# Kernel tuning notes

Measured on AMD Instinct MI355X. Metric: run time of the kernel, lower is better.

The kernel has to match this reference:

```python
import jax, jax.numpy as jnp
import numpy as np

THRESH = 0.5  # original code thresholds raw span logit channel 0 at 0.5


def setup_inputs() -> dict:
    key = jax.random.key(0)
    ks = jax.random.split(key, 9)
    B, S, H, P = 4, 256, 768, 54  # P = num_spo_patterns + 1
    scale = 0.02
    return {
        "sequence_output": jax.random.normal(ks[0], (B, S, H), jnp.float32),
        "W1s": jax.random.normal(ks[1], (H, H), jnp.float32) * scale,
        "b1s": jnp.zeros((H,), jnp.float32),
        "W2s": jax.random.normal(ks[2], (2, H), jnp.float32) * scale,
        "b2s": jnp.zeros((2,), jnp.float32),
        "Wp1": jax.random.normal(ks[3], (H, 2 * H), jnp.float32) * scale,
        "bp1": jnp.zeros((H,), jnp.float32),
        "Wp2": jax.random.normal(ks[4], (P, H), jnp.float32) * scale,
        "bp2": jnp.zeros((P,), jnp.float32),
    }


def reference(sequence_output, W1s, b1s, W2s, b2s, Wp1, bp1, Wp2, bp2):
    x = sequence_output                                # [B,S,H]
    B, S, H = x.shape
    # span classifier: Linear -> ReLU -> Linear
    h = jax.nn.relu(jnp.einsum('bsh,kh->bsk', x, W1s) + b1s)
    span_logits = jnp.einsum('bsh,kh->bsk', h, W2s) + b2s   # [B,S,2]
    cand = span_logits[..., 0] > THRESH                      # [B,S] candidates
    # spo pattern classifier on concat pairs: Linear(2H,H) splits into two H->H maps
    Wa, Wb = Wp1[:, :H], Wp1[:, H:]                          # subject / object halves
    ha = jnp.einsum('bsh,kh->bsk', x, Wa)                    # [B,S,H]
    hb = jnp.einsum('bsh,kh->bsk', x, Wb)                    # [B,S,H]
    pair_hidden = jax.nn.relu(ha[:, :, None, :] + hb[:, None, :, :] + bp1)  # [B,S,S,H]
    pair_logits = jnp.einsum('bijh,ph->bijp', pair_hidden, Wp2) + bp2       # [B,S,S,P]
    # valid pairs: both are candidates and subj != obj (diagonal excluded)
    not_diag = ~jnp.eye(S, dtype=bool)
    valid = cand[:, :, None] & cand[:, None, :] & not_diag   # [B,S,S]
    # dense masked equivalent of the per-pair Python loop (invalid pairs zeroed,
    # matching the zeros fallback for empty candidate sets)
    spo_pattern_logits = jnp.where(valid[..., None], pair_logits, 0.0)
    return spo_pattern_logits
```

## Files before the change

### kernel.cpp

```cpp
#include <hip/hip_runtime.h>
#include <hip/hip_bf16.h>


#define M_ROWS 1024
#define HDIM 768
#define PDIM 54
#define MAXC 256
#define KCHUNK 16
#define NKC (HDIM / KCHUNK)
#define KSPLIT 4
#define KSEG (HDIM / KSPLIT)

#define CANDCNT_OFF  0
#define PAIRCNT_OFF  4
#define CANDIDX_OFF  8192
#define CANDSLOT_OFF 12288
#define PAIR_OFF     16384
#define HPART_OFF    1064960

__global__ __launch_bounds__(256) void gemm_k_kernel(
    const float* __restrict__ x, const float* __restrict__ W1,
    float* __restrict__ hpart, int* __restrict__ counters)
{
    __shared__ float As[16][68];
    __shared__ float Bs[16][68];

    if (blockIdx.x == 0 && blockIdx.y == 0 && blockIdx.z == 0 && threadIdx.x < 2)
        counters[threadIdx.x] = 0;

    const int m0 = blockIdx.x * 64;
    const int n0 = blockIdx.y * 64;
    const int kb = blockIdx.z * KSEG;
    const int t  = threadIdx.x;
    const int tm = t & 15;
    const int tn = t >> 4;
    const int r  = t >> 2;
    const int c4 = (t & 3) * 4;

    float acc[4][4] = {};

    for (int k0 = kb; k0 < kb + KSEG; k0 += 16) {
        float4 av = *(const float4*)(x  + (size_t)(m0 + r) * HDIM + k0 + c4);
        float4 bv = *(const float4*)(W1 + (size_t)(n0 + r) * HDIM + k0 + c4);
        As[c4+0][r] = av.x; As[c4+1][r] = av.y; As[c4+2][r] = av.z; As[c4+3][r] = av.w;
        Bs[c4+0][r] = bv.x; Bs[c4+1][r] = bv.y; Bs[c4+2][r] = bv.z; Bs[c4+3][r] = bv.w;
        __syncthreads();
        #pragma unroll
        for (int kk = 0; kk < 16; ++kk) {
            float a[4], b[4];
            #pragma unroll
            for (int i = 0; i < 4; ++i) a[i] = As[kk][tm * 4 + i];
            #pragma unroll
            for (int j = 0; j < 4; ++j) b[j] = Bs[kk][tn * 4 + j];
            #pragma unroll
            for (int i = 0; i < 4; ++i)
                #pragma unroll
                for (int j = 0; j < 4; ++j)
                    acc[i][j] += a[i] * b[j];
        }
        __syncthreads();
    }

    float* dst = hpart + (size_t)blockIdx.z * (M_ROWS * HDIM);
    #pragma unroll
    for (int i = 0; i < 4; ++i) {
        float4 v = make_float4(acc[i][0], acc[i][1], acc[i][2], acc[i][3]);
        *(float4*)(dst + (size_t)(m0 + tm * 4 + i) * HDIM + n0 + tn * 4) = v;
    }
}

__global__ __launch_bounds__(256) void span_cand_kernel(
    const float* __restrict__ hpart, const float* __restrict__ b1,
    const float* __restrict__ w2row, const float* __restrict__ b2,
    int* __restrict__ candCount, int* __restrict__ candIdx,
    int* __restrict__ candSlot)
{
    const int m = blockIdx.x;
    const int t = threadIdx.x;
    float p = 0.f;
    for (int n = t; n < HDIM; n += 256) {
        float v = hpart[(size_t)m * HDIM + n]
                + hpart[(size_t)(M_ROWS * HDIM) + (size_t)m * HDIM + n]
                + hpart[(size_t)(2 * M_ROWS * HDIM) + (size_t)m * HDIM + n]
                + hpart[(size_t)(3 * M_ROWS * HDIM) + (size_t)m * HDIM + n];
        v += b1[n];
        v = v > 0.f ? v : 0.f;
        p += v * w2row[n];
    }
    __shared__ float wred[4];
    #pragma unroll
    for (int off = 32; off > 0; off >>= 1) p += __shfl_down(p, off, 64);
    if ((t & 63) == 0) wred[t >> 6] = p;
    __syncthreads();
    if (t == 0) {
        float s = wred[0] + wred[1] + wred[2] + wred[3] + b2[0];
        if (s > 0.5f) {
            int sl = atomicAdd(candCount, 1);
            if (sl < MAXC) { candIdx[sl] = m; candSlot[m] = sl; }
            else candSlot[m] = -1;
        } else {
            candSlot[m] = -1;
        }
    }
}

__global__ __launch_bounds__(256) void hab_kernel(
    const float* __restrict__ x, const float* __restrict__ Wp1,
    const int* __restrict__ candCount, const int* __restrict__ candIdx,
    float* __restrict__ ha, float* __restrict__ hb)
{
    __shared__ float xs[HDIM];
    __shared__ float red[2][KCHUNK][17];
    int nc = *candCount; if (nc > MAXC) nc = MAXC;
    const int nitems = nc * NKC;
    const int kk  = threadIdx.x >> 4;
    const int hb0 = (threadIdx.x & 15) * 4;

    for (int item = blockIdx.x; item < nitems; item += gridDim.x) {
        int slot = item / NKC;
        int kc   = item % NKC;
        int row  = candIdx[slot];

        for (int h = threadIdx.x; h < HDIM; h += 256)
            xs[h] = x[(size_t)row * HDIM + h];
        __syncthreads();

        int k = kc * KCHUNK + kk;
        const float* wr = Wp1 + (size_t)k * (2 * HDIM);
        float sa = 0.f, sb = 0.f;
        #pragma unroll
        for (int h = hb0; h < HDIM; h += 64) {
            float4 xv = *(const float4*)(xs + h);
            float4 wa = *(const float4*)(wr + h);
            float4 wb = *(const float4*)(wr + HDIM + h);
            sa += xv.x * wa.x + xv.y * wa.y + xv.z * wa.z + xv.w * wa.w;
            sb += xv.x * wb.x + xv.y * wb.y + xv.z * wb.z + xv.w * wb.w;
        }
        red[0][kk][threadIdx.x & 15] = sa;
        red[1][kk][threadIdx.x & 15] = sb;
        __syncthreads();

        if (threadIdx.x < 32) {
            int which = threadIdx.x >> 4;
            int kk2   = threadIdx.x & 15;
            float s = 0.f;
            #pragma unroll
            for (int g = 0; g < 16; ++g) s += red[which][kk2][g];
            float* dst = which == 0 ? ha : hb;
            dst[(size_t)slot * HDIM + kc * KCHUNK + kk2] = s;
        }
        __syncthreads();
    }
}

__global__ void pairs_kernel(const int* __restrict__ candSlot,
                             int* __restrict__ pairCount, int* __restrict__ pairList)
{
    int idx = blockIdx.x * 256 + threadIdx.x;
    int b = idx >> 16;
    int i = (idx >> 8) & 255;
    int j = idx & 255;
    if (i == j) return;
    if (candSlot[b * 256 + i] >= 0 && candSlot[b * 256 + j] >= 0) {
        int p = atomicAdd(pairCount, 1);
        pairList[p] = idx;
    }
}

__global__ __launch_bounds__(256) void pair_kernel(
    const float* __restrict__ ha, const float* __restrict__ hb,
    const float* __restrict__ bp1, const float* __restrict__ Wp2,
    const float* __restrict__ bp2, const int* __restrict__ candSlot,
    const int* __restrict__ pairCount, const int* __restrict__ pairList,
    float* __restrict__ out)
{
    __shared__ float v[HDIM];
    __shared__ float red[4][PDIM + 2];
    const int np = *pairCount;
    const int t = threadIdx.x;
    for (int p = blockIdx.x; p < np; p += gridDim.x) {
        int idx = pairList[p];
        int b = idx >> 16;
        int i = (idx >> 8) & 255;
        int j = idx & 255;
        int si = candSlot[b * 256 + i];
        int sj = candSlot[b * 256 + j];
        if (t < 192) {
            float4 a4 = *(const float4*)(ha + (size_t)si * HDIM + t * 4);
            float4 b4 = *(const float4*)(hb + (size_t)sj * HDIM + t * 4);
            float4 c4 = *(const float4*)(bp1 + t * 4);
            float4 r;
            r.x = a4.x + b4.x + c4.x; r.x = r.x > 0.f ? r.x : 0.f;
            r.y = a4.y + b4.y + c4.y; r.y = r.y > 0.f ? r.y : 0.f;
            r.z = a4.z + b4.z + c4.z; r.z = r.z > 0.f ? r.z : 0.f;
            r.w = a4.w + b4.w + c4.w; r.w = r.w > 0.f ? r.w : 0.f;
            *(float4*)(v + t * 4) = r;
        }
        __syncthreads();
        if (t < 216) {
            int pp  = t % PDIM;
            int seg = t / PDIM;
            const float* w = Wp2 + (size_t)pp * HDIM + seg * 192;
            const float* vv = v + seg * 192;
            float s = 0.f;
            for (int h = 0; h < 192; h += 4) {
                float4 a = *(const float4*)(vv + h);
                float4 b2_ = *(const float4*)(w + h);
                s += a.x * b2_.x + a.y * b2_.y + a.z * b2_.z + a.w * b2_.w;
            }
            red[seg][pp] = s;
        }
        __syncthreads();
        if (t < PDIM)
            out[(size_t)idx * PDIM + t] = red[0][t] + red[1][t] + red[2][t] + red[3][t] + bp2[t];
        __syncthreads();
    }
}

extern "C" void kernel_launch(void* const* d_in, const int* in_sizes, int n_in,
                              void* d_out, int out_size, void* d_ws, size_t ws_size,
                              hipStream_t stream) {
    const float* x   = (const float*)d_in[0];
    const float* W1s = (const float*)d_in[1];
    const float* b1s = (const float*)d_in[2];
    const float* W2s = (const float*)d_in[3];
    const float* b2s = (const float*)d_in[4];
    const float* Wp1 = (const float*)d_in[5];
    const float* bp1 = (const float*)d_in[6];
    const float* Wp2 = (const float*)d_in[7];
    const float* bp2 = (const float*)d_in[8];

    char* ws = (char*)d_ws;
    int*   counters = (int*)(ws + CANDCNT_OFF);
    int*   candCnt  = counters;
    int*   pairCnt  = counters + 1;
    int*   candIdx  = (int*)(ws + CANDIDX_OFF);
    int*   candSlot = (int*)(ws + CANDSLOT_OFF);
    int*   pairList = (int*)(ws + PAIR_OFF);
    float* hpart    = (float*)(ws + HPART_OFF);
    float* ha       = hpart + (size_t)KSPLIT * M_ROWS * HDIM;
    float* hb       = ha + (size_t)MAXC * HDIM;
    float* out = (float*)d_out;

    hipMemsetAsync(out, 0, (size_t)out_size * sizeof(float), stream);

    dim3 g(M_ROWS / 64, HDIM / 64, KSPLIT);
    gemm_k_kernel<<<g, 256, 0, stream>>>(x, W1s, hpart, counters);

    span_cand_kernel<<<M_ROWS, 256, 0, stream>>>(hpart, b1s, W2s, b2s,
                                                 candCnt, candIdx, candSlot);

    hab_kernel<<<2048, 256, 0, stream>>>(x, Wp1, candCnt, candIdx, ha, hb);

    pairs_kernel<<<1024, 256, 0, stream>>>(candSlot, pairCnt, pairList);

    pair_kernel<<<512, 256, 0, stream>>>(ha, hb, bp1, Wp2, bp2,
                                         candSlot, pairCnt, pairList, out);
}
```

Measured before the change: 138.9 us.

## Fuse pair enumeration and output zeroing into the pair logits kernel

Drops the separate pairs_kernel and the output memset. Each pair_kernel block now owns a fixed 512-pair slice of the output: it zeroes that slice, builds its own valid-pair list in shared memory with a local atomic, then computes logits for those pairs. This removes two launches, the global atomic counter and the global pair list. The cost is that work is no longer spread round-robin across blocks, so clustered candidates could unbalance the load.

```diff
diff --git a/kernel.cpp b/kernel.cpp
--- a/kernel.cpp
+++ b/kernel.cpp
@@ -12,10 +12,8 @@
 #define KSEG (HDIM / KSPLIT)
 
 #define CANDCNT_OFF  0
-#define PAIRCNT_OFF  4
 #define CANDIDX_OFF  8192
 #define CANDSLOT_OFF 12288
-#define PAIR_OFF     16384
 #define HPART_OFF    1064960
 
 __global__ __launch_bounds__(256) void gemm_k_kernel(
@@ -25,8 +23,8 @@
     __shared__ float As[16][68];
     __shared__ float Bs[16][68];
 
-    if (blockIdx.x == 0 && blockIdx.y == 0 && blockIdx.z == 0 && threadIdx.x < 2)
-        counters[threadIdx.x] = 0;
+    if (blockIdx.x == 0 && blockIdx.y == 0 && blockIdx.z == 0 && threadIdx.x == 0)
+        counters[0] = 0;
 
     const int m0 = blockIdx.x * 64;
     const int n0 = blockIdx.y * 64;
@@ -153,33 +151,43 @@
     }
 }
 
-__global__ void pairs_kernel(const int* __restrict__ candSlot,
-                             int* __restrict__ pairCount, int* __restrict__ pairList)
-{
-    int idx = blockIdx.x * 256 + threadIdx.x;
-    int b = idx >> 16;
-    int i = (idx >> 8) & 255;
-    int j = idx & 255;
-    if (i == j) return;
-    if (candSlot[b * 256 + i] >= 0 && candSlot[b * 256 + j] >= 0) {
-        int p = atomicAdd(pairCount, 1);
-        pairList[p] = idx;
-    }
-}
-
 __global__ __launch_bounds__(256) void pair_kernel(
     const float* __restrict__ ha, const float* __restrict__ hb,
     const float* __restrict__ bp1, const float* __restrict__ Wp2,
     const float* __restrict__ bp2, const int* __restrict__ candSlot,
-    const int* __restrict__ pairCount, const int* __restrict__ pairList,
     float* __restrict__ out)
 {
+    __shared__ int plist[512];
+    __shared__ int pcnt;
     __shared__ float v[HDIM];
     __shared__ float red[4][PDIM + 2];
-    const int np = *pairCount;
     const int t = threadIdx.x;
-    for (int p = blockIdx.x; p < np; p += gridDim.x) {
-        int idx = pairList[p];
+
+    float* outb = out + (size_t)blockIdx.x * 512 * PDIM;
+    float4 z = make_float4(0.f, 0.f, 0.f, 0.f);
+    #pragma unroll
+    for (int q = 0; q < 27; ++q)
+        *(float4*)(outb + (size_t)(q * 256 + t) * 4) = z;
+
+    if (t == 0) pcnt = 0;
+    __syncthreads();
+
+    #pragma unroll
+    for (int q = 0; q < 2; ++q) {
+        int idx = blockIdx.x * 512 + q * 256 + t;
+        int b = idx >> 16;
+        int i = (idx >> 8) & 255;
+        int j = idx & 255;
+        if (i != j && candSlot[b * 256 + i] >= 0 && candSlot[b * 256 + j] >= 0) {
+            int p = atomicAdd(&pcnt, 1);
+            plist[p] = idx;
+        }
+    }
+    __syncthreads();
+    const int np = pcnt;
+
+    for (int p = 0; p < np; ++p) {
+        int idx = plist[p];
         int b = idx >> 16;
         int i = (idx >> 8) & 255;
         int j = idx & 255;
@@ -233,17 +241,13 @@
     char* ws = (char*)d_ws;
     int*   counters = (int*)(ws + CANDCNT_OFF);
     int*   candCnt  = counters;
-    int*   pairCnt  = counters + 1;
     int*   candIdx  = (int*)(ws + CANDIDX_OFF);
     int*   candSlot = (int*)(ws + CANDSLOT_OFF);
-    int*   pairList = (int*)(ws + PAIR_OFF);
     float* hpart    = (float*)(ws + HPART_OFF);
     float* ha       = hpart + (size_t)KSPLIT * M_ROWS * HDIM;
     float* hb       = ha + (size_t)MAXC * HDIM;
     float* out = (float*)d_out;
 
-    hipMemsetAsync(out, 0, (size_t)out_size * sizeof(float), stream);
-
     dim3 g(M_ROWS / 64, HDIM / 64, KSPLIT);
     gemm_k_kernel<<<g, 256, 0, stream>>>(x, W1s, hpart, counters);
 
@@ -252,8 +256,5 @@
 
     hab_kernel<<<2048, 256, 0, stream>>>(x, Wp1, candCnt, candIdx, ha, hb);
 
-    pairs_kernel<<<1024, 256, 0, stream>>>(candSlot, pairCnt, pairList);
-
-    pair_kernel<<<512, 256, 0, stream>>>(ha, hb, bp1, Wp2, bp2,
-                                         candSlot, pairCnt, pairList, out);
-}
+    pair_kernel<<<512, 256, 0, stream>>>(ha, hb, bp1, Wp2, bp2, candSlot, out);
+}
```

Result: slower. 146.4 us (+5.4%).
